# Performance work log

Hardware: AMD Instinct MI355X
Metric: run time of the kernel (lower is better)

Reference implementation:

```python
import jax, jax.numpy as jnp
import numpy as np

N, V, H, K = 65536, 200, 128, 32

def _corr_cols(a, B):
    # Pearson correlation between vector a [M] and each column of B [M, V]
    ac = a - a.mean()
    Bc = B - B.mean(axis=0)
    num = (ac[:, None] * Bc).sum(axis=0)
    den = jnp.sqrt((ac ** 2).sum() * (Bc ** 2).sum(axis=0))
    return jnp.nan_to_num(num / den, nan=0.0)

def _pairwise_features(tv, ti, cv, ci):
    # tv, ti: [N]; cv, ci: [N, V] -> features [V, 11]
    tvc = tv[:, None]
    both = (1.0 - ti)[:, None] * (1.0 - ci)
    n = both.sum(0) + 1e-8
    tmean = (tvc * both).sum(0) / n
    cmean = (cv * both).sum(0) / n
    tcent = (tvc - tmean) * both
    ccent = (cv - cmean) * both
    cov = (tcent * ccent).sum(0) / n
    tstd = jnp.sqrt((tcent ** 2).sum(0) / n + 1e-8)
    cstd = jnp.sqrt((ccent ** 2).sum(0) / n + 1e-8)
    corr = cov / (tstd * cstd + 1e-8)
    mi = -0.5 * jnp.log(1.0 - jnp.minimum(corr ** 2, 0.99) + 1e-8)
    tmin, tmax = tv.min(), tv.max()
    cmin, cmax = cv.min(0), cv.max(0)
    overlap = jnp.maximum(0.0, (jnp.minimum(tmax, cmax) - jnp.maximum(tmin, cmin)) / (jnp.maximum(tmax - tmin, cmax - cmin) + 1e-8))
    lag = _corr_cols(tv[1:], cv[:-1])       # corrcoef(candidate[:-1], target[1:])
    rev = _corr_cols(tv[:-1], cv[1:])       # corrcoef(target[:-1], candidate[1:])
    var_t = jnp.var(tv)
    coef = corr * jnp.std(tv) / (cv.std(0) + 1e-8)
    residual = tvc - coef * (cv - cv.mean(0))
    var_ratio = residual.var(0) / (var_t + 1e-8)
    intv = (ci > 0.5).astype(tv.dtype)
    t_int = (tvc * intv).sum(0) / (intv.sum(0) + 1e-8)
    t_no = (tvc * (1.0 - intv)).sum(0) / ((1.0 - intv).sum(0) + 1e-8)
    effect = jnp.abs(t_int - t_no)
    tr = jnp.argsort(jnp.argsort(tv)).astype(tv.dtype)
    cr = jnp.argsort(jnp.argsort(cv, axis=0), axis=0).astype(tv.dtype)
    rank_corr = _corr_cols(tr, cr)
    feats = jnp.stack([corr, jnp.abs(corr), corr ** 2, mi, overlap, effect,
                       rank_corr, jnp.sign(corr), lag, rev, var_ratio], axis=-1)
    return jnp.nan_to_num(feats, nan=0.0)

def _forward(target_embedding, node_embeddings, data, W_pair, b_pair, Wq, bq, Wk, bk,
             W1, b1, ln_scale, ln_offset, W2, b2, W3, b3, Wd, target_idx):
    n_vars = node_embeddings.shape[0]
    tv, ti = data[:, target_idx, 0], data[:, target_idx, 1]
    cv, ci = data[:, :, 0], data[:, :, 1]
    pf = _pairwise_features(tv, ti, cv, ci)                       # [V, 11]
    pf = jnp.where((jnp.arange(n_vars) == target_idx)[:, None], 0.0, pf)
    q = target_embedding @ Wq + bq                                # [K]
    k = node_embeddings @ Wk + bk + (pf @ W_pair + b_pair)        # [V, K]
    scores = (k @ q) / jnp.sqrt(jnp.asarray(float(K), dtype=q.dtype))
    te = jnp.broadcast_to(target_embedding, (n_vars, target_embedding.shape[0]))
    combined = jnp.concatenate([te, node_embeddings, pf * 10.0], axis=-1)  # [V, 2H+11]
    h = jax.nn.gelu(combined @ W1 + b1)
    mu = h.mean(-1, keepdims=True)
    var = ((h - mu) ** 2).mean(-1, keepdims=True)
    h = (h - mu) / jnp.sqrt(var + 1e-5) * ln_scale + ln_offset    # LayerNorm (haiku eps=1e-5)
    h = jax.nn.gelu(h @ W2 + b2)
    net = (h @ W3 + b3)[:, 0]
    direct = (pf[:, jnp.array([0, 8, 10])] @ Wd)[:, 0]
    return scores + net + 0.5 * direct

def setup_inputs():
    key = jax.random.key(0)
    ks = jax.random.split(key, 16)
    def vs_uniform(k, fan_in, shape):
        # hk.initializers.VarianceScaling(2.0, 'fan_in', 'uniform')
        lim = np.sqrt(6.0 / fan_in)
        return jax.random.uniform(k, shape, minval=-lim, maxval=lim, dtype=jnp.float32)
    vals = jax.random.normal(ks[0], (N, V), dtype=jnp.float32)
    intv = (jax.random.uniform(ks[1], (N, V)) < 0.1).astype(jnp.float32)
    data = jnp.stack([vals, intv, jnp.ones((N, V), jnp.float32)], axis=-1)  # [N, V, 3]
    return {
        'target_embedding': jax.random.normal(ks[2], (H,), dtype=jnp.float32),
        'node_embeddings': jax.random.normal(ks[3], (V, H), dtype=jnp.float32),
        'data': data,
        'W_pair': vs_uniform(ks[4], 11, (11, K)), 'b_pair': jnp.zeros((K,), jnp.float32),
        'Wq': vs_uniform(ks[5], H, (H, K)), 'bq': jnp.zeros((K,), jnp.float32),
        'Wk': vs_uniform(ks[6], H, (H, K)), 'bk': jnp.zeros((K,), jnp.float32),
        'W1': vs_uniform(ks[7], 2 * H + 11, (2 * H + 11, H)), 'b1': jnp.zeros((H,), jnp.float32),
        'ln_scale': jnp.ones((H,), jnp.float32), 'ln_offset': jnp.zeros((H,), jnp.float32),
        'W2': vs_uniform(ks[8], H, (H, H // 2)), 'b2': jnp.zeros((H // 2,), jnp.float32),
        'W3': vs_uniform(ks[9], H // 2, (H // 2, 1)), 'b3': jnp.zeros((1,), jnp.float32),
        'Wd': vs_uniform(ks[10], 3, (3, 1)),
        'target_idx': 0,
    }

def reference(target_embedding, node_embeddings, data, W_pair, b_pair, Wq, bq, Wk, bk,
              W1, b1, ln_scale, ln_offset, W2, b2, W3, b3, Wd, target_idx):
    return _forward(target_embedding, node_embeddings, data, W_pair, b_pair, Wq, bq, Wk, bk,
                    W1, b1, ln_scale, ln_offset, W2, b2, W3, b3, Wd, target_idx)
```

## Files before the change

### kernel.cpp

```cpp
#include <hip/hip_runtime.h>
#include <stdint.h>

#define N_ROWS 65536
#define NV 200
#define NH 128
#define NKD 32
#define NBKT 32768
#define ROWS_B 64
#define NBLK (N_ROWS/ROWS_B)

__device__ __forceinline__ uint32_t fkey(float x){
  uint32_t u = __float_as_uint(x);
  return (u & 0x80000000u) ? ~u : (u | 0x80000000u);
}

__global__ __launch_bounds__(256) void k_extract(
    const float* __restrict__ data, const int* __restrict__ tgt,
    float* __restrict__ tvArr, float* __restrict__ tiArr,
    unsigned int* __restrict__ histT, double* __restrict__ tvP){
  int i = blockIdx.x*256 + threadIdx.x;
  int tg = *tgt;
  float v  = data[(size_t)i*600 + tg*3 + 0];
  float ti = data[(size_t)i*600 + tg*3 + 1];
  tvArr[i] = v; tiArr[i] = ti;
  atomicAdd(&histT[fkey(v)>>17], 1u);
  double s = (double)v, ss = (double)v*(double)v;
  float mn = v, mx = v;
  for (int off=32; off; off>>=1){
    s  += __shfl_down(s,  off);
    ss += __shfl_down(ss, off);
    mn = fminf(mn, __shfl_down(mn, off));
    mx = fmaxf(mx, __shfl_down(mx, off));
  }
  __shared__ double sd[4][4];
  int w = threadIdx.x >> 6;
  if ((threadIdx.x & 63) == 0){ sd[w][0]=s; sd[w][1]=ss; sd[w][2]=mn; sd[w][3]=mx; }
  __syncthreads();
  if (threadIdx.x == 0){
    double S=0, SS=0, MN=sd[0][2], MX=sd[0][3];
    for (int q=0;q<4;q++){ S+=sd[q][0]; SS+=sd[q][1]; MN=fmin(MN,sd[q][2]); MX=fmax(MX,sd[q][3]); }
    double* p = tvP + (size_t)blockIdx.x*4;
    p[0]=S; p[1]=SS; p[2]=MN; p[3]=MX;
  }
}

__global__ __launch_bounds__(256) void k_scan(unsigned int* __restrict__ histT){
  __shared__ unsigned int h[256*129];
  __shared__ unsigned int aux[256];
  int t = threadIdx.x;
  for (int idx=t; idx<NBKT; idx+=256) h[(idx>>7)*129 + (idx&127)] = histT[idx];
  __syncthreads();
  unsigned int s = 0;
  #pragma unroll 8
  for (int k=0;k<128;k++) s += h[t*129+k];
  aux[t] = s; __syncthreads();
  for (int off=1; off<256; off<<=1){
    unsigned int v = (t>=off) ? aux[t-off] : 0u;
    __syncthreads();
    aux[t] += v;
    __syncthreads();
  }
  unsigned int run = aux[t] - s;
  #pragma unroll 8
  for (int k=0;k<128;k++){
    unsigned int c = h[t*129+k];
    h[t*129+k] = __float_as_uint((float)run + 0.5f*((float)c - 1.f));
    run += c;
  }
  __syncthreads();
  for (int idx=t; idx<NBKT; idx+=256) histT[idx] = h[(idx>>7)*129 + (idx&127)];
}

__global__ __launch_bounds__(256, 4) void k_main(
    const float* __restrict__ data, const float* __restrict__ tvArr,
    const float* __restrict__ tiArr, uint16_t* __restrict__ bktT,
    float* __restrict__ colP){
  int t = threadIdx.x, blk = blockIdx.x;
  int i0 = blk*ROWS_B;
  bool act = (t < NV);
  const float* base = data + (size_t)i0*600 + t*3;
  uint16_t* bout = bktT + (size_t)t*N_ROWS + i0;

  float facc[13];
  #pragma unroll
  for (int s=0;s<13;s++) facc[s]=0.f;
  float cmin = 3.4e38f, cmax = -3.4e38f;

  for (int c=0; c<4; ++c){
    int r0 = i0 + c*16;
    float2 v[16];
    if (act){
      #pragma unroll
      for (int r=0;r<16;r++)
        v[r] = *(const float2*)(base + (size_t)(c*16+r)*600);
    }
    float tvv[18];
    #pragma unroll
    for (int k=0;k<18;k++){
      int i = r0 + k - 1;
      tvv[k] = (i>=0 && i<N_ROWS) ? tvArr[i] : 0.f;
    }
    float tii[16];
    #pragma unroll
    for (int k=0;k<16;k++) tii[k] = tiArr[r0+k];

    if (act){
      uint16_t bb[16];
      #pragma unroll
      for (int r=0;r<16;r++){
        float cv = v[r].x;
        float ci = v[r].y;
        float tv = tvv[r+1], tvm = tvv[r], tvp = tvv[r+2];
        float b  = (1.f-tii[r])*(1.f-ci);
        facc[0]+=cv;        facc[1]+=cv*cv;     facc[2]+=tv*cv;
        facc[3]+=ci;        facc[4]+=tv*ci;
        facc[5]+=b;         facc[6]+=tv*b;      facc[7]+=cv*b;
        facc[8]+=tv*cv*b;   facc[9]+=tv*tv*b;   facc[10]+=cv*cv*b;
        facc[11]+=tvp*cv;   facc[12]+=tvm*cv;
        cmin = fminf(cmin, cv); cmax = fmaxf(cmax, cv);
        bb[r] = (uint16_t)(fkey(cv)>>17);
      }
      *((uint4*)(bout + c*16))     = *((uint4*)(bb));
      *((uint4*)(bout + c*16 + 8)) = *((uint4*)(bb + 8));
    }
  }
  if (act){
    float* dst = colP + ((size_t)t*NBLK + blk)*16;
    #pragma unroll
    for (int s=0;s<13;s++) dst[s] = facc[s];
    dst[13]=cmin; dst[14]=cmax;
  }
}

__global__ __launch_bounds__(256) void k_comb_cols(const float* __restrict__ colP,
                                                   double* __restrict__ colStats){
  int j = blockIdx.x, t = threadIdx.x;
  double a[13];
  #pragma unroll
  for (int s=0;s<13;s++) a[s]=0.0;
  float mn = 3.4e38f, mx = -3.4e38f;
  for (int b=t; b<NBLK; b+=256){
    const float* p = colP + ((size_t)j*NBLK + b)*16;
    #pragma unroll
    for (int s=0;s<13;s++) a[s] += (double)p[s];
    mn = fminf(mn, p[13]); mx = fmaxf(mx, p[14]);
  }
  for (int off=32; off; off>>=1){
    #pragma unroll
    for (int s=0;s<13;s++) a[s] += __shfl_down(a[s], off);
    mn = fminf(mn, __shfl_down(mn, off));
    mx = fmaxf(mx, __shfl_down(mx, off));
  }
  __shared__ double sd[4][15];
  int w = t >> 6;
  if ((t & 63) == 0){
    #pragma unroll
    for (int s=0;s<13;s++) sd[w][s]=a[s];
    sd[w][13]=(double)mn; sd[w][14]=(double)mx;
  }
  __syncthreads();
  if (t == 0){
    double* d = colStats + (size_t)j*16;
    #pragma unroll
    for (int s=0;s<13;s++) d[s] = sd[0][s]+sd[1][s]+sd[2][s]+sd[3][s];
    double MN=sd[0][13], MX=sd[0][14];
    for (int q=1;q<4;q++){ MN=fmin(MN,sd[q][13]); MX=fmax(MX,sd[q][14]); }
    d[13]=MN; d[14]=MX;
  }
}

__global__ __launch_bounds__(1024, 1) void k_rank(const uint16_t* __restrict__ bktT,
                                                  const float* __restrict__ tvArr,
                                                  const unsigned int* __restrict__ histT,
                                                  double* __restrict__ colStats){
  __shared__ unsigned int h[1024*33];
  __shared__ unsigned int aux[1024];
  __shared__ double daux[16];
  int t = threadIdx.x, j = blockIdx.x;
  const uint16_t* col = bktT + (size_t)j*N_ROWS;
  for (int idx=t; idx<1024*33; idx+=1024) h[idx]=0u;
  __syncthreads();
  for (int k=0;k<N_ROWS/1024;k++){
    int b = (int)col[t + k*1024];
    atomicAdd(&h[(b>>5)*33 + (b&31)], 1u);
  }
  __syncthreads();
  unsigned int s = 0;
  #pragma unroll 8
  for (int k=0;k<32;k++) s += h[t*33+k];
  aux[t]=s; __syncthreads();
  for (int off=1; off<1024; off<<=1){
    unsigned int v = (t>=off) ? aux[t-off] : 0u;
    __syncthreads();
    aux[t] += v;
    __syncthreads();
  }
  unsigned int run = aux[t] - s;
  #pragma unroll 8
  for (int k=0;k<32;k++){
    unsigned int c = h[t*33+k];
    h[t*33+k] = __float_as_uint((float)run + 0.5f*((float)c - 1.f));
    run += c;
  }
  __syncthreads();
  double srr = 0.0;
  for (int k=0;k<N_ROWS/1024;k++){
    int i = t + k*1024;
    int b = (int)col[i];
    float tr = __uint_as_float(histT[fkey(tvArr[i])>>17]);
    srr += (double)tr * (double)__uint_as_float(h[(b>>5)*33 + (b&31)]);
  }
  for (int off=32; off; off>>=1) srr += __shfl_down(srr, off);
  if ((t&63)==0) daux[t>>6] = srr;
  __syncthreads();
  if (t==0){
    double s16=0;
    for (int q=0;q<16;q++) s16 += daux[q];
    colStats[(size_t)j*16 + 15] = s16;
  }
}

__device__ __forceinline__ float gelu_t(float x){
  float x3 = x*x*x;
  return 0.5f*x*(1.f + tanhf(0.7978845608f*(x + 0.044715f*x3)));
}

__global__ __launch_bounds__(128) void k_head(
    const float* __restrict__ te, const float* __restrict__ ne, const float* __restrict__ data,
    const float* __restrict__ Wpair, const float* __restrict__ bpair,
    const float* __restrict__ Wq, const float* __restrict__ bq,
    const float* __restrict__ Wk, const float* __restrict__ bk,
    const float* __restrict__ W1, const float* __restrict__ b1,
    const float* __restrict__ lns, const float* __restrict__ lno,
    const float* __restrict__ W2, const float* __restrict__ b2,
    const float* __restrict__ W3, const float* __restrict__ b3,
    const float* __restrict__ Wd, const int* __restrict__ tgt,
    const double* __restrict__ colStats, const double* __restrict__ tvP,
    const float* __restrict__ tvArr, float* __restrict__ out){
  int j = blockIdx.x, t = threadIdx.x;
  int tg = *tgt;

  __shared__ double tvsd[2][4];
  {
    double s  = tvP[t*4+0] + tvP[(t+128)*4+0];
    double ss = tvP[t*4+1] + tvP[(t+128)*4+1];
    double mn = fmin(tvP[t*4+2], tvP[(t+128)*4+2]);
    double mx = fmax(tvP[t*4+3], tvP[(t+128)*4+3]);
    for (int off=32; off; off>>=1){
      s  += __shfl_down(s,  off);
      ss += __shfl_down(ss, off);
      mn = fmin(mn, __shfl_down(mn, off));
      mx = fmax(mx, __shfl_down(mx, off));
    }
    int w = t>>6;
    if ((t&63)==0){ tvsd[w][0]=s; tvsd[w][1]=ss; tvsd[w][2]=mn; tvsd[w][3]=mx; }
    __syncthreads();
  }
  double S_t  = tvsd[0][0] + tvsd[1][0];
  double S_tt = tvsd[0][1] + tvsd[1][1];
  float tmin  = (float)fmin(tvsd[0][2], tvsd[1][2]);
  float tmax  = (float)fmax(tvsd[0][3], tvsd[1][3]);

  const double* cs = colStats + (size_t)j*16;
  double S_c=cs[0], S_cc=cs[1], S_tc=cs[2], S_ci=cs[3], S_ti=cs[4], S_b=cs[5],
         S_tb=cs[6], S_cb=cs[7], S_tcb=cs[8], S_ttb=cs[9], S_ccb=cs[10], L=cs[11], R=cs[12];
  float cmin=(float)cs[13], cmax=(float)cs[14];
  double S_rr=cs[15];
  float tv0=tvArr[0], tvN=tvArr[N_ROWS-1];
  float cv0=data[j*3], cvN=data[(size_t)(N_ROWS-1)*600 + j*3];
  const double Nd = (double)N_ROWS;
  double n = S_b + 1e-8;
  double tmean=S_tb/n, cmean=S_cb/n;
  double cov=(S_tcb - tmean*S_cb - cmean*S_tb + tmean*cmean*S_b)/n;
  double t2=S_ttb - 2.0*tmean*S_tb + tmean*tmean*S_b;
  double c2=S_ccb - 2.0*cmean*S_cb + cmean*cmean*S_b;
  double tstd=sqrt(t2/n + 1e-8), cstd=sqrt(c2/n + 1e-8);
  double corr = cov/(tstd*cstd + 1e-8);
  double mi = -0.5*log(1.0 - fmin(corr*corr, 0.99) + 1e-8);
  float ovn = fminf(tmax,cmax) - fmaxf(tmin,cmin);
  float ovd = fmaxf(tmax-tmin, cmax-cmin) + 1e-8f;
  float overlap = fmaxf(0.f, ovn/ovd);
  double M = Nd - 1.0;
  double Sa=S_t-(double)tv0, Saa=S_tt-(double)tv0*(double)tv0;
  double Sb2=S_c-(double)cvN, Sbb=S_cc-(double)cvN*(double)cvN;
  double lnum = L - Sa*Sb2/M;
  double lden2 = (Saa - Sa*Sa/M)*(Sbb - Sb2*Sb2/M);
  double lag = (lden2 > 0.0) ? lnum/sqrt(lden2) : 0.0;
  double Sa2=S_t-(double)tvN, Saa2=S_tt-(double)tvN*(double)tvN;
  double Sc2=S_c-(double)cv0, Scc2=S_cc-(double)cv0*(double)cv0;
  double rnum = R - Sa2*Sc2/M;
  double rden2 = (Saa2 - Sa2*Sa2/M)*(Scc2 - Sc2*Sc2/M);
  double rev = (rden2 > 0.0) ? rnum/sqrt(rden2) : 0.0;
  double var_t = S_tt/Nd - (S_t/Nd)*(S_t/Nd);
  double var_c = S_cc/Nd - (S_c/Nd)*(S_c/Nd);
  double coef = corr*sqrt(var_t)/(sqrt(var_c) + 1e-8);
  double covf = S_tc/Nd - (S_t/Nd)*(S_c/Nd);
  double var_res = var_t + coef*coef*var_c - 2.0*coef*covf;
  double var_ratio = var_res/(var_t + 1e-8);
  double t_int = S_ti/(S_ci + 1e-8);
  double t_no  = (S_t - S_ti)/((Nd - S_ci) + 1e-8);
  double effect = fabs(t_int - t_no);
  const double m_ = (Nd-1.0)*0.5;
  double rank_corr = (S_rr - Nd*m_*m_) / (Nd*(Nd*Nd-1.0)/12.0);
  float pf[11];
  pf[0]=(float)corr; pf[1]=(float)fabs(corr); pf[2]=(float)(corr*corr); pf[3]=(float)mi;
  pf[4]=overlap; pf[5]=(float)effect; pf[6]=(float)rank_corr;
  pf[7]=(float)((corr>0.0)-(corr<0.0)); pf[8]=(float)lag; pf[9]=(float)rev; pf[10]=(float)var_ratio;
  if (j == tg){
    #pragma unroll
    for (int q=0;q<11;q++) pf[q]=0.f;
  }
  const float* nej = ne + (size_t)j*NH;
  float h = b1[t];
  for (int e=0;e<NH;e++) h += te[e]*W1[e*NH + t];
  for (int e=0;e<NH;e++) h += nej[e]*W1[(NH+e)*NH + t];
  #pragma unroll
  for (int f=0;f<11;f++) h += 10.f*pf[f]*W1[(2*NH+f)*NH + t];
  h = gelu_t(h);
  __shared__ float redW[2];
  __shared__ float hnS[NH];
  __shared__ float h2S[64];
  float v = h;
  for (int off=32; off; off>>=1) v += __shfl_down(v, off);
  if ((t&63)==0) redW[t>>6]=v;
  __syncthreads();
  float mu = (redW[0]+redW[1])*(1.f/128.f);
  __syncthreads();
  float d = h - mu;
  v = d*d;
  for (int off=32; off; off>>=1) v += __shfl_down(v, off);
  if ((t&63)==0) redW[t>>6]=v;
  __syncthreads();
  float var = (redW[0]+redW[1])*(1.f/128.f);
  float hn = d/sqrtf(var + 1e-5f)*lns[t] + lno[t];
  hnS[t] = hn;
  __syncthreads();
  if (t < 64){
    float h2 = b2[t];
    for (int o=0;o<NH;o++) h2 += hnS[o]*W2[o*64 + t];
    h2S[t] = gelu_t(h2);
  }
  __syncthreads();
  float netv = 0.f, scv = 0.f;
  if (t < 64){
    float v2 = h2S[t]*W3[t];
    for (int off=32; off; off>>=1) v2 += __shfl_down(v2, off);
    if (t==0) netv = v2 + b3[0];
  }
  if (t < 32){
    float q = bq[t], k = bk[t] + bpair[t];
    for (int e=0;e<NH;e++){ q += te[e]*Wq[e*NKD + t]; k += nej[e]*Wk[e*NKD + t]; }
    #pragma unroll
    for (int f=0;f<11;f++) k += pf[f]*Wpair[f*NKD + t];
    float sc = k*q;
    for (int off=16; off; off>>=1) sc += __shfl_down(sc, off, 32);
    if (t==0) scv = sc/sqrtf(32.f);
  }
  if (t == 0){
    float direct = pf[0]*Wd[0] + pf[8]*Wd[1] + pf[10]*Wd[2];
    out[j] = scv + netv + 0.5f*direct;
  }
}

extern "C" void kernel_launch(void* const* d_in, const int* in_sizes, int n_in,
                              void* d_out, int out_size, void* d_ws, size_t ws_size,
                              hipStream_t stream) {
  const float* te    = (const float*)d_in[0];
  const float* ne    = (const float*)d_in[1];
  const float* data  = (const float*)d_in[2];
  const float* Wpair = (const float*)d_in[3];
  const float* bpair = (const float*)d_in[4];
  const float* Wq    = (const float*)d_in[5];
  const float* bq    = (const float*)d_in[6];
  const float* Wk    = (const float*)d_in[7];
  const float* bk    = (const float*)d_in[8];
  const float* W1    = (const float*)d_in[9];
  const float* b1    = (const float*)d_in[10];
  const float* lns   = (const float*)d_in[11];
  const float* lno   = (const float*)d_in[12];
  const float* W2    = (const float*)d_in[13];
  const float* b2    = (const float*)d_in[14];
  const float* W3    = (const float*)d_in[15];
  const float* b3    = (const float*)d_in[16];
  const float* Wd    = (const float*)d_in[17];
  const int*   tgt   = (const int*)d_in[18];
  float* out = (float*)d_out;

  char* ws = (char*)d_ws;
  size_t off = 0;
  auto alloc = [&](size_t bytes)->char*{
    char* p = ws + off;
    off = (off + bytes + 255) & ~(size_t)255;
    return p;
  };
  uint16_t*     bktT     = (uint16_t*)    alloc((size_t)NV*N_ROWS*2);
  float*        tvArr    = (float*)       alloc(N_ROWS*4);
  float*        tiArr    = (float*)       alloc(N_ROWS*4);
  unsigned int* histT    = (unsigned int*)alloc(NBKT*4);
  double*       tvP      = (double*)      alloc(256*4*8);
  float*        colP     = (float*)       alloc((size_t)NV*NBLK*16*4);
  double*       colStats = (double*)      alloc((size_t)NV*16*8);
  if (off > ws_size) return;

  hipMemsetAsync(histT, 0, NBKT*4, stream);
  k_extract<<<dim3(N_ROWS/256), dim3(256), 0, stream>>>(data, tgt, tvArr, tiArr, histT, tvP);
  k_scan<<<dim3(1), dim3(256), 0, stream>>>(histT);
  k_main<<<dim3(NBLK), dim3(256), 0, stream>>>(data, tvArr, tiArr, bktT, colP);
  k_comb_cols<<<dim3(NV), dim3(256), 0, stream>>>(colP, colStats);
  k_rank<<<dim3(NV), dim3(1024), 0, stream>>>(bktT, tvArr, histT, colStats);
  k_head<<<dim3(NV), dim3(128), 0, stream>>>(te, ne, data, Wpair, bpair, Wq, bq, Wk, bk,
                                             W1, b1, lns, lno, W2, b2, W3, b3, Wd, tgt,
                                             colStats, tvP, tvArr, out);
}
```

Baseline: 434.2 us.

## Fuse column-stat combine into rank kernel and precompute target ranks

Removes the separate k_comb_cols launch by having each of k_rank's 1024 threads load one block partial (NBLK=1024) and reduce it before building the histogram. Adds a small k_trank kernel that computes the target's rank values once, so k_rank no longer does a per-row histT gather in every column block. k_main now buffers all 64 bucket indices per thread and writes them with eight 16-byte stores at the end. The cost is more registers in k_main and an extra tiny launch.

```diff
diff --git a/kernel.cpp b/kernel.cpp
--- a/kernel.cpp
+++ b/kernel.cpp
@@ -71,6 +71,13 @@
   for (int idx=t; idx<NBKT; idx+=256) histT[idx] = h[(idx>>7)*129 + (idx&127)];
 }
 
+__global__ __launch_bounds__(256) void k_trank(const float* __restrict__ tvArr,
+                                               const unsigned int* __restrict__ histT,
+                                               float* __restrict__ trArr){
+  int i = blockIdx.x*256 + threadIdx.x;
+  trArr[i] = __uint_as_float(histT[fkey(tvArr[i])>>17]);
+}
+
 __global__ __launch_bounds__(256, 4) void k_main(
     const float* __restrict__ data, const float* __restrict__ tvArr,
     const float* __restrict__ tiArr, uint16_t* __restrict__ bktT,
@@ -79,13 +86,14 @@
   int i0 = blk*ROWS_B;
   bool act = (t < NV);
   const float* base = data + (size_t)i0*600 + t*3;
-  uint16_t* bout = bktT + (size_t)t*N_ROWS + i0;
 
   float facc[13];
   #pragma unroll
   for (int s=0;s<13;s++) facc[s]=0.f;
   float cmin = 3.4e38f, cmax = -3.4e38f;
-
+  uint16_t bb[ROWS_B];
+
+  #pragma unroll
   for (int c=0; c<4; ++c){
     int r0 = i0 + c*16;
     float2 v[16];
@@ -105,7 +113,6 @@
     for (int k=0;k<16;k++) tii[k] = tiArr[r0+k];
 
     if (act){
-      uint16_t bb[16];
       #pragma unroll
       for (int r=0;r<16;r++){
         float cv = v[r].x;
@@ -118,13 +125,14 @@
         facc[8]+=tv*cv*b;   facc[9]+=tv*tv*b;   facc[10]+=cv*cv*b;
         facc[11]+=tvp*cv;   facc[12]+=tvm*cv;
         cmin = fminf(cmin, cv); cmax = fmaxf(cmax, cv);
-        bb[r] = (uint16_t)(fkey(cv)>>17);
+        bb[c*16+r] = (uint16_t)(fkey(cv)>>17);
       }
-      *((uint4*)(bout + c*16))     = *((uint4*)(bb));
-      *((uint4*)(bout + c*16 + 8)) = *((uint4*)(bb + 8));
     }
   }
   if (act){
+    uint4* bo = (uint4*)(bktT + (size_t)t*N_ROWS + i0);
+    #pragma unroll
+    for (int q=0;q<8;q++) bo[q] = ((const uint4*)bb)[q];
     float* dst = colP + ((size_t)t*NBLK + blk)*16;
     #pragma unroll
     for (int s=0;s<13;s++) dst[s] = facc[s];
@@ -132,54 +140,51 @@
   }
 }
 
-__global__ __launch_bounds__(256) void k_comb_cols(const float* __restrict__ colP,
-                                                   double* __restrict__ colStats){
-  int j = blockIdx.x, t = threadIdx.x;
-  double a[13];
-  #pragma unroll
-  for (int s=0;s<13;s++) a[s]=0.0;
-  float mn = 3.4e38f, mx = -3.4e38f;
-  for (int b=t; b<NBLK; b+=256){
-    const float* p = colP + ((size_t)j*NBLK + b)*16;
-    #pragma unroll
-    for (int s=0;s<13;s++) a[s] += (double)p[s];
-    mn = fminf(mn, p[13]); mx = fmaxf(mx, p[14]);
-  }
-  for (int off=32; off; off>>=1){
-    #pragma unroll
-    for (int s=0;s<13;s++) a[s] += __shfl_down(a[s], off);
-    mn = fminf(mn, __shfl_down(mn, off));
-    mx = fmaxf(mx, __shfl_down(mx, off));
-  }
-  __shared__ double sd[4][15];
-  int w = t >> 6;
-  if ((t & 63) == 0){
-    #pragma unroll
-    for (int s=0;s<13;s++) sd[w][s]=a[s];
-    sd[w][13]=(double)mn; sd[w][14]=(double)mx;
-  }
-  __syncthreads();
-  if (t == 0){
-    double* d = colStats + (size_t)j*16;
-    #pragma unroll
-    for (int s=0;s<13;s++) d[s] = sd[0][s]+sd[1][s]+sd[2][s]+sd[3][s];
-    double MN=sd[0][13], MX=sd[0][14];
-    for (int q=1;q<4;q++){ MN=fmin(MN,sd[q][13]); MX=fmax(MX,sd[q][14]); }
-    d[13]=MN; d[14]=MX;
-  }
-}
-
 __global__ __launch_bounds__(1024, 1) void k_rank(const uint16_t* __restrict__ bktT,
-                                                  const float* __restrict__ tvArr,
-                                                  const unsigned int* __restrict__ histT,
+                                                  const float* __restrict__ trArr,
+                                                  const float* __restrict__ colP,
                                                   double* __restrict__ colStats){
   __shared__ unsigned int h[1024*33];
   __shared__ unsigned int aux[1024];
   __shared__ double daux[16];
+  __shared__ double sdc[16][15];
   int t = threadIdx.x, j = blockIdx.x;
   const uint16_t* col = bktT + (size_t)j*N_ROWS;
   for (int idx=t; idx<1024*33; idx+=1024) h[idx]=0u;
-  __syncthreads();
+
+  {
+    const float* p = colP + ((size_t)j*NBLK + t)*16;
+    double a[13];
+    #pragma unroll
+    for (int s=0;s<13;s++) a[s] = (double)p[s];
+    float mn = p[13], mx = p[14];
+    for (int off=32; off; off>>=1){
+      #pragma unroll
+      for (int s=0;s<13;s++) a[s] += __shfl_down(a[s], off);
+      mn = fminf(mn, __shfl_down(mn, off));
+      mx = fmaxf(mx, __shfl_down(mx, off));
+    }
+    int w = t >> 6;
+    if ((t & 63) == 0){
+      #pragma unroll
+      for (int s=0;s<13;s++) sdc[w][s]=a[s];
+      sdc[w][13]=(double)mn; sdc[w][14]=(double)mx;
+    }
+    __syncthreads();
+    if (t == 0){
+      double* d = colStats + (size_t)j*16;
+      #pragma unroll
+      for (int s=0;s<13;s++){
+        double acc=0;
+        for (int q=0;q<16;q++) acc += sdc[q][s];
+        d[s]=acc;
+      }
+      double MN=sdc[0][13], MX=sdc[0][14];
+      for (int q=1;q<16;q++){ MN=fmin(MN,sdc[q][13]); MX=fmax(MX,sdc[q][14]); }
+      d[13]=MN; d[14]=MX;
+    }
+  }
+
   for (int k=0;k<N_ROWS/1024;k++){
     int b = (int)col[t + k*1024];
     atomicAdd(&h[(b>>5)*33 + (b&31)], 1u);
@@ -207,8 +212,7 @@
   for (int k=0;k<N_ROWS/1024;k++){
     int i = t + k*1024;
     int b = (int)col[i];
-    float tr = __uint_as_float(histT[fkey(tvArr[i])>>17]);
-    srr += (double)tr * (double)__uint_as_float(h[(b>>5)*33 + (b&31)]);
+    srr += (double)trArr[i] * (double)__uint_as_float(h[(b>>5)*33 + (b&31)]);
   }
   for (int off=32; off; off>>=1) srr += __shfl_down(srr, off);
   if ((t&63)==0) daux[t>>6] = srr;
@@ -396,6 +400,7 @@
   uint16_t*     bktT     = (uint16_t*)    alloc((size_t)NV*N_ROWS*2);
   float*        tvArr    = (float*)       alloc(N_ROWS*4);
   float*        tiArr    = (float*)       alloc(N_ROWS*4);
+  float*        trArr    = (float*)       alloc(N_ROWS*4);
   unsigned int* histT    = (unsigned int*)alloc(NBKT*4);
   double*       tvP      = (double*)      alloc(256*4*8);
   float*        colP     = (float*)       alloc((size_t)NV*NBLK*16*4);
@@ -405,9 +410,9 @@
   hipMemsetAsync(histT, 0, NBKT*4, stream);
   k_extract<<<dim3(N_ROWS/256), dim3(256), 0, stream>>>(data, tgt, tvArr, tiArr, histT, tvP);
   k_scan<<<dim3(1), dim3(256), 0, stream>>>(histT);
+  k_trank<<<dim3(N_ROWS/256), dim3(256), 0, stream>>>(tvArr, histT, trArr);
   k_main<<<dim3(NBLK), dim3(256), 0, stream>>>(data, tvArr, tiArr, bktT, colP);
-  k_comb_cols<<<dim3(NV), dim3(256), 0, stream>>>(colP, colStats);
-  k_rank<<<dim3(NV), dim3(1024), 0, stream>>>(bktT, tvArr, histT, colStats);
+  k_rank<<<dim3(NV), dim3(1024), 0, stream>>>(bktT, trArr, colP, colStats);
   k_head<<<dim3(NV), dim3(128), 0, stream>>>(te, ne, data, Wpair, bpair, Wq, bq, Wk, bk,
                                              W1, b1, lns, lno, W2, b2, W3, b3, Wd, tgt,
                                              colStats, tvP, tvArr, out);
```

Measured after the change: 393.2 us. 1.1x faster.
